# Optimization experiments

Measured on AMD Instinct MI355X. Metric: run time of the kernel, lower is better.

The kernel has to match this reference:

```python
import jax, jax.numpy as jnp
import numpy as np

HIDDEN = 2048
NUM_HEADS = 16
HEAD_DIM = HIDDEN // NUM_HEADS  # 128
SCALE = HEAD_DIM ** -0.5


def setup_inputs() -> dict:
    key = jax.random.key(0)
    ks = jax.random.split(key, 5)
    B, S = 2, 2048
    init = HIDDEN ** -0.5  # roughly kaiming-uniform scale for Linear weights
    return {
        "hidden_states": jax.random.normal(ks[0], (B, S, HIDDEN), dtype=jnp.float32),
        "Wq": jax.random.normal(ks[1], (HIDDEN, HIDDEN), dtype=jnp.float32) * init,
        "Wk": jax.random.normal(ks[2], (HIDDEN, HIDDEN), dtype=jnp.float32) * init,
        "Wv": jax.random.normal(ks[3], (HIDDEN, HIDDEN), dtype=jnp.float32) * init,
        "Wo": jax.random.normal(ks[4], (HIDDEN, HIDDEN), dtype=jnp.float32) * init,
    }


def reference(hidden_states, Wq, Wk, Wv, Wo):
    B, S, _ = hidden_states.shape
    # Projections (nn.Linear: x @ W.T; weights stored as [out, in])
    q = (hidden_states @ Wq.T).reshape(B, S, NUM_HEADS, HEAD_DIM).transpose(0, 2, 1, 3)
    k = (hidden_states @ Wk.T).reshape(B, S, NUM_HEADS, HEAD_DIM).transpose(0, 2, 1, 3)
    v = (hidden_states @ Wv.T).reshape(B, S, NUM_HEADS, HEAD_DIM).transpose(0, 2, 1, 3)
    # Full quadratic attention (faithful to the source's explicit materialization)
    scores = jnp.einsum("bhqd,bhkd->bhqk", q, k) * SCALE  # [B,H,S,S]
    probs = jax.nn.softmax(scores, axis=-1)
    attn = jnp.einsum("bhqk,bhkd->bhqd", probs, v)  # [B,H,S,Dh]
    attn = attn.transpose(0, 2, 1, 3).reshape(B, S, HIDDEN)
    return attn @ Wo.T
```

## Files before the change

kernel.cpp:

```cpp
#include <hip/hip_runtime.h>
#include <cstdint>

#define HIDDEN 2048
#define NHEADS 16
#define DH 128
#define BATCH 2
#define SEQ 2048
#define MTOT 4096
#define BH (BATCH * NHEADS)

typedef __attribute__((ext_vector_type(8))) short bf16x8;
typedef __attribute__((ext_vector_type(4))) float f32x4;

static constexpr float QSCALE = (float)(0.08838834764831845 * 1.4426950408889634);

__device__ __forceinline__ unsigned short f2bf(float f) {
  union { float f; uint32_t u; } v; v.f = f;
  uint32_t r = v.u + 0x7FFFu + ((v.u >> 16) & 1u);
  return (unsigned short)(r >> 16);
}
__device__ __forceinline__ uint32_t cvtpk(float lo, float hi) {
  uint32_t r;
  asm("v_cvt_pk_bf16_f32 %0, %1, %2" : "=v"(r) : "v"(lo), "v"(hi));
  return r;
}
__device__ __forceinline__ f32x4 mfma16(bf16x8 a, bf16x8 b, f32x4 c) {
  return __builtin_amdgcn_mfma_f32_16x16x32_bf16(a, b, c, 0, 0, 0);
}

typedef const __attribute__((address_space(1))) unsigned char* gas1_t;
typedef __attribute__((address_space(3))) unsigned char* las3_t;
__device__ __forceinline__ void gll16(const void* g, void* l) {
  __builtin_amdgcn_global_load_lds((gas1_t)g, (las3_t)l, 16, 0, 0);
}

__global__ __launch_bounds__(256) void cast_all(
    const float* __restrict__ X, const float* __restrict__ Wq,
    const float* __restrict__ Wk, const float* __restrict__ Wv,
    const float* __restrict__ Wo, unsigned short* __restrict__ Xb,
    unsigned short* __restrict__ Wqb, unsigned short* __restrict__ Wkb,
    unsigned short* __restrict__ Wvb, unsigned short* __restrict__ Wob) {
  const int n1 = MTOT * HIDDEN;
  const int i = (blockIdx.x * 256 + threadIdx.x) * 4;
  const float* s;
  unsigned short* d;
  int o;
  if (i < n1) {
    s = X; d = Xb; o = i;
  } else {
    const int j = i - n1;
    const int w = j >> 22;
    o = j & ((1 << 22) - 1);
    s = (w == 0) ? Wq : (w == 1) ? Wk : (w == 2) ? Wv : Wo;
    d = (w == 0) ? Wqb : (w == 1) ? Wkb : (w == 2) ? Wvb : Wob;
  }
  float4 f = *(const float4*)&s[o];
  ushort4 u;
  u.x = f2bf(f.x); u.y = f2bf(f.y); u.z = f2bf(f.z); u.w = f2bf(f.w);
  *(ushort4*)&d[o] = u;
}

template <int VM, bool PF>
__device__ __forceinline__ void qkv3_body(
    int t, char* SM, const unsigned short* aS, const unsigned short* bSq,
    const unsigned short* bSk, const unsigned short* bSv, int wv, int wr,
    int wc, int g, int lr, f32x4 (&accQ)[4][2], f32x4 (&accK)[4][2],
    f32x4 (&accV)[4][2]) {
  const char* slot = SM + (t % 3) * 32768;
  char* slot2 = SM + ((t + 2) % 3) * 32768;
  const size_t ko = (size_t)(t + 2) * 32;
  const int coff = (g ^ ((lr >> 1) & 3)) * 16;
  bf16x8 a[4], bq[2], bk[2], bv[2];
#pragma unroll
  for (int mi = 0; mi < 4; ++mi)
    a[mi] = *(const bf16x8*)(slot + (wr * 64 + mi * 16 + lr) * 64 + coff);
#pragma unroll
  for (int ni = 0; ni < 2; ++ni) {
    const int brow = (wc * 32 + ni * 16 + lr) * 64 + coff;
    bq[ni] = *(const bf16x8*)(slot + 8192 + brow);
    bk[ni] = *(const bf16x8*)(slot + 16384 + brow);
    bv[ni] = *(const bf16x8*)(slot + 24576 + brow);
  }
  if (PF) {
    gll16(aS + ko, slot2 + wv * 1024);
    gll16(bSq + ko, slot2 + 8192 + wv * 1024);
    gll16(bSk + ko, slot2 + 16384 + wv * 1024);
    gll16(bSv + ko, slot2 + 24576 + wv * 1024);
  }
  __builtin_amdgcn_s_setprio(1);
#pragma unroll
  for (int mi = 0; mi < 4; ++mi)
#pragma unroll
    for (int ni = 0; ni < 2; ++ni) {
      accQ[mi][ni] = mfma16(a[mi], bq[ni], accQ[mi][ni]);
      accK[mi][ni] = mfma16(a[mi], bk[ni], accK[mi][ni]);
      accV[mi][ni] = mfma16(a[mi], bv[ni], accV[mi][ni]);
    }
  __builtin_amdgcn_s_setprio(0);
  if (VM == 4) asm volatile("s_waitcnt vmcnt(4)" ::: "memory");
  else if (VM == 0) asm volatile("s_waitcnt vmcnt(0)" ::: "memory");
  if (VM >= 0) __builtin_amdgcn_s_barrier();
}

__global__ __launch_bounds__(512) void gemm_qkv_fused(
    const unsigned short* __restrict__ A, const unsigned short* __restrict__ Wq,
    const unsigned short* __restrict__ Wk, const unsigned short* __restrict__ Wv,
    unsigned short* __restrict__ Qb, unsigned short* __restrict__ Kb,
    unsigned short* __restrict__ Vb) {
  __shared__ __align__(16) char SM[98304];
  const int tid = threadIdx.x;
  const int lane = tid & 63, wv = tid >> 6;
  const int wr = wv >> 2, wc = wv & 3;
  const int g = lane >> 4, lr = lane & 15;
  const int m0 = blockIdx.y * 128, n0 = blockIdx.x * 128;

  const int row0 = tid >> 2, j0 = (tid & 3) ^ ((row0 >> 1) & 3);
  const unsigned short* aS  = A  + (size_t)(m0 + row0) * HIDDEN + j0 * 8;
  const unsigned short* bSq = Wq + (size_t)(n0 + row0) * HIDDEN + j0 * 8;
  const unsigned short* bSk = Wk + (size_t)(n0 + row0) * HIDDEN + j0 * 8;
  const unsigned short* bSv = Wv + (size_t)(n0 + row0) * HIDDEN + j0 * 8;

  f32x4 accQ[4][2], accK[4][2], accV[4][2];
#pragma unroll
  for (int i = 0; i < 4; ++i)
#pragma unroll
    for (int j = 0; j < 2; ++j) {
      accQ[i][j] = (f32x4){0.f, 0.f, 0.f, 0.f};
      accK[i][j] = (f32x4){0.f, 0.f, 0.f, 0.f};
      accV[i][j] = (f32x4){0.f, 0.f, 0.f, 0.f};
    }

#pragma unroll
  for (int tt = 0; tt < 2; ++tt) {
    char* slot = SM + tt * 32768;
    const size_t ko = (size_t)tt * 32;
    gll16(aS + ko, slot + wv * 1024);
    gll16(bSq + ko, slot + 8192 + wv * 1024);
    gll16(bSk + ko, slot + 16384 + wv * 1024);
    gll16(bSv + ko, slot + 24576 + wv * 1024);
  }
  asm volatile("s_waitcnt vmcnt(4)" ::: "memory");
  __builtin_amdgcn_s_barrier();

  for (int t = 0; t < 62; ++t)
    qkv3_body<4, true>(t, SM, aS, bSq, bSk, bSv, wv, wr, wc, g, lr,
                       accQ, accK, accV);
  qkv3_body<0, false>(62, SM, aS, bSq, bSk, bSv, wv, wr, wc, g, lr,
                      accQ, accK, accV);
  qkv3_body<-1, false>(63, SM, aS, bSq, bSk, bSv, wv, wr, wc, g, lr,
                       accQ, accK, accV);

#pragma unroll
  for (int mi = 0; mi < 4; ++mi)
#pragma unroll
    for (int ni = 0; ni < 2; ++ni)
#pragma unroll
      for (int r = 0; r < 4; ++r) {
        const int row = m0 + wr * 64 + mi * 16 + g * 4 + r;
        const int col = n0 + wc * 32 + ni * 16 + lr;
        const int b = row >> 11, s = row & (SEQ - 1);
        const int h = col >> 7, d = col & (DH - 1);
        const size_t base = (size_t)(b * NHEADS + h) * SEQ * DH;
        Qb[base + (size_t)s * DH + d] = f2bf(accQ[mi][ni][r] * QSCALE);
        Kb[base + (size_t)(s >> 5) * 4096 + (d >> 3) * 256 + (s & 31) * 8 + (d & 7)] =
            f2bf(accK[mi][ni][r]);
        Vb[base + (size_t)(s >> 3) * 1024 + d * 8 + (s & 7)] =
            f2bf(accV[mi][ni][r]);
      }
}

template <int VM, bool PF>
__device__ __forceinline__ void pipe_body(
    int kt, char* SM, const unsigned short* aS0, const unsigned short* aS1,
    const unsigned short* bS0, const unsigned short* bS1,
    const unsigned short* bS2, const unsigned short* bS3, int wv, int wr,
    int wc, int g, int lr, f32x4 (&acc)[4][4]) {
  const char* Ac = SM + (kt % 3) * 49152;
  const char* Bc = Ac + 16384;
  char* slot2 = SM + ((kt + 2) % 3) * 49152;
  const size_t ko = (size_t)(kt + 2) * 64;
  const int rx = lr & 7;
  bf16x8 a0[4], b0[4], a1[4], b1[4];
#pragma unroll
  for (int mi = 0; mi < 4; ++mi)
    a0[mi] = *(const bf16x8*)(Ac + (wr * 64 + mi * 16 + lr) * 128 + ((g ^ rx) * 16));
#pragma unroll
  for (int ni = 0; ni < 4; ++ni)
    b0[ni] = *(const bf16x8*)(Bc + (wc * 64 + ni * 16 + lr) * 128 + ((g ^ rx) * 16));
  if (PF) {
    gll16(aS0 + ko, slot2 + wv * 2048);
    gll16(aS1 + ko, slot2 + wv * 2048 + 1024);
    gll16(bS0 + ko, slot2 + 16384 + wv * 4096);
    gll16(bS1 + ko, slot2 + 16384 + wv * 4096 + 1024);
    gll16(bS2 + ko, slot2 + 16384 + wv * 4096 + 2048);
    gll16(bS3 + ko, slot2 + 16384 + wv * 4096 + 3072);
  }
#pragma unroll
  for (int mi = 0; mi < 4; ++mi)
    a1[mi] = *(const bf16x8*)(Ac + (wr * 64 + mi * 16 + lr) * 128 + (((4 + g) ^ rx) * 16));
#pragma unroll
  for (int ni = 0; ni < 4; ++ni)
    b1[ni] = *(const bf16x8*)(Bc + (wc * 64 + ni * 16 + lr) * 128 + (((4 + g) ^ rx) * 16));
  __builtin_amdgcn_s_setprio(1);
#pragma unroll
  for (int mi = 0; mi < 4; ++mi)
#pragma unroll
    for (int ni = 0; ni < 4; ++ni)
      acc[mi][ni] = mfma16(a0[mi], b0[ni], acc[mi][ni]);
#pragma unroll
  for (int mi = 0; mi < 4; ++mi)
#pragma unroll
    for (int ni = 0; ni < 4; ++ni)
      acc[mi][ni] = mfma16(a1[mi], b1[ni], acc[mi][ni]);
  __builtin_amdgcn_s_setprio(0);
  if (VM == 6) asm volatile("s_waitcnt vmcnt(6)" ::: "memory");
  else if (VM == 0) asm volatile("s_waitcnt vmcnt(0)" ::: "memory");
  if (VM >= 0) __builtin_amdgcn_s_barrier();
}

__global__ __launch_bounds__(512) void gemm_out_pipe(
    const unsigned short* __restrict__ A, const unsigned short* __restrict__ W,
    float* __restrict__ C) {
  __shared__ __align__(16) char SM[147456];
  const int tid = threadIdx.x;
  const int lane = tid & 63, wv = tid >> 6;
  const int wr = wv >> 2, wc = wv & 3;
  const int g = lane >> 4, lr = lane & 15;
  const int m0 = blockIdx.y * 128, n0 = blockIdx.x * 256;

  const int idxA0 = wv * 128 + lane, idxA1 = idxA0 + 64;
  const int rA0 = idxA0 >> 3, cA0 = (idxA0 & 7) ^ (rA0 & 7);
  const int rA1 = idxA1 >> 3, cA1 = (idxA1 & 7) ^ (rA1 & 7);
  const unsigned short* aS0 = A + (size_t)(m0 + rA0) * HIDDEN + cA0 * 8;
  const unsigned short* aS1 = A + (size_t)(m0 + rA1) * HIDDEN + cA1 * 8;
  const int idxB0 = wv * 256 + lane, idxB1 = idxB0 + 64,
            idxB2 = idxB0 + 128, idxB3 = idxB0 + 192;
  const int rB0 = idxB0 >> 3, cB0 = (idxB0 & 7) ^ (rB0 & 7);
  const int rB1 = idxB1 >> 3, cB1 = (idxB1 & 7) ^ (rB1 & 7);
  const int rB2 = idxB2 >> 3, cB2 = (idxB2 & 7) ^ (rB2 & 7);
  const int rB3 = idxB3 >> 3, cB3 = (idxB3 & 7) ^ (rB3 & 7);
  const unsigned short* bS0 = W + (size_t)(n0 + rB0) * HIDDEN + cB0 * 8;
  const unsigned short* bS1 = W + (size_t)(n0 + rB1) * HIDDEN + cB1 * 8;
  const unsigned short* bS2 = W + (size_t)(n0 + rB2) * HIDDEN + cB2 * 8;
  const unsigned short* bS3 = W + (size_t)(n0 + rB3) * HIDDEN + cB3 * 8;

  f32x4 acc[4][4];
#pragma unroll
  for (int i = 0; i < 4; ++i)
#pragma unroll
    for (int j = 0; j < 4; ++j) acc[i][j] = (f32x4){0.f, 0.f, 0.f, 0.f};

#pragma unroll
  for (int tt = 0; tt < 2; ++tt) {
    char* slot = SM + tt * 49152;
    const size_t ko = (size_t)tt * 64;
    gll16(aS0 + ko, slot + wv * 2048);
    gll16(aS1 + ko, slot + wv * 2048 + 1024);
    gll16(bS0 + ko, slot + 16384 + wv * 4096);
    gll16(bS1 + ko, slot + 16384 + wv * 4096 + 1024);
    gll16(bS2 + ko, slot + 16384 + wv * 4096 + 2048);
    gll16(bS3 + ko, slot + 16384 + wv * 4096 + 3072);
  }
  asm volatile("s_waitcnt vmcnt(6)" ::: "memory");
  __builtin_amdgcn_s_barrier();

  for (int kt = 0; kt < 30; ++kt)
    pipe_body<6, true>(kt, SM, aS0, aS1, bS0, bS1, bS2, bS3, wv, wr, wc, g,
                       lr, acc);
  pipe_body<0, false>(30, SM, aS0, aS1, bS0, bS1, bS2, bS3, wv, wr, wc, g,
                      lr, acc);
  pipe_body<-1, false>(31, SM, aS0, aS1, bS0, bS1, bS2, bS3, wv, wr, wc, g,
                       lr, acc);

#pragma unroll
  for (int mi = 0; mi < 4; ++mi)
#pragma unroll
    for (int ni = 0; ni < 4; ++ni)
#pragma unroll
      for (int r = 0; r < 4; ++r) {
        const int row = m0 + wr * 64 + mi * 16 + g * 4 + r;
        const int col = n0 + wc * 64 + ni * 16 + lr;
        C[(size_t)row * HIDDEN + col] = acc[mi][ni][r];
      }
}

__global__ __launch_bounds__(256, 4) void attn_mfma(const unsigned short* __restrict__ Q,
                                                    const unsigned short* __restrict__ K,
                                                    const unsigned short* __restrict__ V,
                                                    unsigned short* __restrict__ Ab) {
  const int bid = blockIdx.x;
  const int bh = bid & 31;
  const int q0 = (bid >> 5) * 64;
  const int tid = threadIdx.x;
  const int wv = tid >> 6, lane = tid & 63;
  const int g = lane >> 4, lr = lane & 15;
  const unsigned short* Qh = Q + (size_t)bh * SEQ * DH;
  const unsigned short* Kh = K + (size_t)bh * SEQ * DH;
  const unsigned short* Vh = V + (size_t)bh * SEQ * DH;

  __shared__ __align__(16) unsigned short Kls[2][4096];
  __shared__ __align__(16) unsigned short Vls[2][4096];
  __shared__ __align__(16) unsigned short Pw[4][16][40];

  bf16x8 qf[4];
#pragma unroll
  for (int kb = 0; kb < 4; ++kb)
    qf[kb] = *(const bf16x8*)&Qh[(size_t)(q0 + wv * 16 + lr) * DH + kb * 32 + g * 8];

  f32x4 acc[8];
#pragma unroll
  for (int dn = 0; dn < 8; ++dn) acc[dn] = (f32x4){0.f, 0.f, 0.f, 0.f};
  float mrun = -1e30f;
  float lrun = 0.f;

#pragma unroll
  for (int j = 0; j < 2; ++j) {
    const int c = j * 256 + tid;
    gll16(Kh + (size_t)c * 8, (char*)&Kls[0][0] + j * 4096 + wv * 1024);
    gll16(Vh + (size_t)c * 8, (char*)&Vls[0][0] + j * 4096 + wv * 1024);
  }

  for (int t = 0; t < 64; ++t) {
    const int cur = t & 1;
    asm volatile("s_waitcnt vmcnt(0)" ::: "memory");
    __builtin_amdgcn_s_barrier();
    if (t + 1 < 64) {
      const unsigned short* Kn = Kh + (size_t)(t + 1) * 4096;
      const unsigned short* Vn = Vh + (size_t)(t + 1) * 4096;
      char* kd = (char*)&Kls[cur ^ 1][0];
      char* vd = (char*)&Vls[cur ^ 1][0];
#pragma unroll
      for (int j = 0; j < 2; ++j) {
        const int c = j * 256 + tid;
        gll16(Kn + (size_t)c * 8, kd + j * 4096 + wv * 1024);
        gll16(Vn + (size_t)c * 8, vd + j * 4096 + wv * 1024);
      }
    }

    const char* Kc = (const char*)&Kls[cur][0];
    const char* Vc = (const char*)&Vls[cur][0];

    f32x4 st0 = (f32x4){0.f, 0.f, 0.f, 0.f};
    f32x4 st1 = (f32x4){0.f, 0.f, 0.f, 0.f};
    __builtin_amdgcn_s_setprio(1);
#pragma unroll
    for (int kb = 0; kb < 4; ++kb) {
      const int cb = (kb * 4 + g) * 32;
      bf16x8 kf0 = *(const bf16x8*)(Kc + (cb + lr) * 16);
      bf16x8 kf1 = *(const bf16x8*)(Kc + (cb + 16 + lr) * 16);
      st0 = mfma16(kf0, qf[kb], st0);
      st1 = mfma16(kf1, qf[kb], st1);
    }
    __builtin_amdgcn_s_setprio(0);
    float mt = fmaxf(fmaxf(fmaxf(st0[0], st0[1]), fmaxf(st0[2], st0[3])),
                     fmaxf(fmaxf(st1[0], st1[1]), fmaxf(st1[2], st1[3])));
    mt = fmaxf(mt, __shfl_xor(mt, 16));
    mt = fmaxf(mt, __shfl_xor(mt, 32));
    if (!__all(mt <= mrun + 8.0f)) {
      const float mnew = fmaxf(mrun, mt);
      const float corr = __builtin_amdgcn_exp2f(mrun - mnew);
      lrun *= corr;
      mrun = mnew;
      const f32x4 cv = (f32x4){__shfl(corr, g * 4 + 0), __shfl(corr, g * 4 + 1),
                               __shfl(corr, g * 4 + 2), __shfl(corr, g * 4 + 3)};
#pragma unroll
      for (int dn = 0; dn < 8; ++dn) acc[dn] *= cv;
    }
    float p[8], ls = 0.f;
#pragma unroll
    for (int r = 0; r < 4; ++r) {
      p[r] = __builtin_amdgcn_exp2f(st0[r] - mrun);
      p[4 + r] = __builtin_amdgcn_exp2f(st1[r] - mrun);
      ls += p[r] + p[4 + r];
    }
    lrun += ls;
    uint2 pk0, pk1;
    pk0.x = cvtpk(p[0], p[1]); pk0.y = cvtpk(p[2], p[3]);
    pk1.x = cvtpk(p[4], p[5]); pk1.y = cvtpk(p[6], p[7]);
    *(uint2*)&Pw[wv][lr][4 * g] = pk0;
    *(uint2*)&Pw[wv][lr][16 + 4 * g] = pk1;
    bf16x8 ap = *(const bf16x8*)&Pw[wv][lr][8 * g];
    __builtin_amdgcn_s_setprio(1);
#pragma unroll
    for (int dn = 0; dn < 8; ++dn) {
      bf16x8 vf = *(const bf16x8*)(Vc + (g * 128 + dn * 16 + lr) * 16);
      acc[dn] = mfma16(ap, vf, acc[dn]);
    }
    __builtin_amdgcn_s_setprio(0);
  }

  const int b = bh >> 4, h = bh & 15;
  lrun += __shfl_xor(lrun, 16);
  lrun += __shfl_xor(lrun, 32);
  const float inv = 1.f / lrun;
  float ir[4];
#pragma unroll
  for (int r = 0; r < 4; ++r) ir[r] = __shfl(inv, g * 4 + r);
#pragma unroll
  for (int dn = 0; dn < 8; ++dn)
#pragma unroll
    for (int r = 0; r < 4; ++r) {
      const int srow = q0 + wv * 16 + g * 4 + r;
      Ab[((size_t)(b * SEQ + srow) * NHEADS + h) * DH + dn * 16 + lr] =
          f2bf(acc[dn][r] * ir[r]);
    }
}

extern "C" void kernel_launch(void* const* d_in, const int* in_sizes, int n_in,
                              void* d_out, int out_size, void* d_ws,
                              size_t ws_size, hipStream_t stream) {
  const float* X  = (const float*)d_in[0];
  const float* Wq = (const float*)d_in[1];
  const float* Wk = (const float*)d_in[2];
  const float* Wv = (const float*)d_in[3];
  const float* Wo = (const float*)d_in[4];
  float* out = (float*)d_out;

  const int n1 = MTOT * HIDDEN;
  const int n2 = HIDDEN * HIDDEN;

  char* p = (char*)d_ws;
  unsigned short* Xb  = (unsigned short*)(p + 0);
  unsigned short* Qb  = (unsigned short*)(p + 16777216);
  unsigned short* Kb  = (unsigned short*)(p + 33554432);
  unsigned short* Vb  = (unsigned short*)(p + 50331648);
  unsigned short* Wqb = (unsigned short*)(p + 67108864);
  unsigned short* Wkb = (unsigned short*)(p + 75497472);
  unsigned short* Wvb = (unsigned short*)(p + 83886080);
  unsigned short* Wob = (unsigned short*)(p + 92274688);
  unsigned short* Ab  = (unsigned short*)(p + 100663296);

  cast_all<<<(n1 + 4 * n2) / 1024, 256, 0, stream>>>(X, Wq, Wk, Wv, Wo, Xb, Wqb,
                                                     Wkb, Wvb, Wob);

  gemm_qkv_fused<<<dim3(HIDDEN / 128, MTOT / 128), 512, 0, stream>>>(
      Xb, Wqb, Wkb, Wvb, Qb, Kb, Vb);

  attn_mfma<<<dim3(1024), 256, 0, stream>>>(Qb, Kb, Vb, Ab);

  gemm_out_pipe<<<dim3(HIDDEN / 256, MTOT / 128), 512, 0, stream>>>(Ab, Wob, out);
}
```

Measured before the change: 272.0 us.

## Switch QKV GEMM from triple-buffered to double-buffered LDS pipeline

Replaces the three-slot LDS ring with prefetch distance two by a simple two-slot double buffer that prefetches one K-tile ahead. Shared memory per block drops from 96KB to 64KB, which may allow more blocks per CU. The cost is a full vmcnt(0) wait and a barrier at the top of every iteration, so global load latency is hidden less.

```diff
diff --git a/kernel.cpp b/kernel.cpp
--- a/kernel.cpp
+++ b/kernel.cpp
@@ -60,54 +60,12 @@
   *(ushort4*)&d[o] = u;
 }
 
-template <int VM, bool PF>
-__device__ __forceinline__ void qkv3_body(
-    int t, char* SM, const unsigned short* aS, const unsigned short* bSq,
-    const unsigned short* bSk, const unsigned short* bSv, int wv, int wr,
-    int wc, int g, int lr, f32x4 (&accQ)[4][2], f32x4 (&accK)[4][2],
-    f32x4 (&accV)[4][2]) {
-  const char* slot = SM + (t % 3) * 32768;
-  char* slot2 = SM + ((t + 2) % 3) * 32768;
-  const size_t ko = (size_t)(t + 2) * 32;
-  const int coff = (g ^ ((lr >> 1) & 3)) * 16;
-  bf16x8 a[4], bq[2], bk[2], bv[2];
-#pragma unroll
-  for (int mi = 0; mi < 4; ++mi)
-    a[mi] = *(const bf16x8*)(slot + (wr * 64 + mi * 16 + lr) * 64 + coff);
-#pragma unroll
-  for (int ni = 0; ni < 2; ++ni) {
-    const int brow = (wc * 32 + ni * 16 + lr) * 64 + coff;
-    bq[ni] = *(const bf16x8*)(slot + 8192 + brow);
-    bk[ni] = *(const bf16x8*)(slot + 16384 + brow);
-    bv[ni] = *(const bf16x8*)(slot + 24576 + brow);
-  }
-  if (PF) {
-    gll16(aS + ko, slot2 + wv * 1024);
-    gll16(bSq + ko, slot2 + 8192 + wv * 1024);
-    gll16(bSk + ko, slot2 + 16384 + wv * 1024);
-    gll16(bSv + ko, slot2 + 24576 + wv * 1024);
-  }
-  __builtin_amdgcn_s_setprio(1);
-#pragma unroll
-  for (int mi = 0; mi < 4; ++mi)
-#pragma unroll
-    for (int ni = 0; ni < 2; ++ni) {
-      accQ[mi][ni] = mfma16(a[mi], bq[ni], accQ[mi][ni]);
-      accK[mi][ni] = mfma16(a[mi], bk[ni], accK[mi][ni]);
-      accV[mi][ni] = mfma16(a[mi], bv[ni], accV[mi][ni]);
-    }
-  __builtin_amdgcn_s_setprio(0);
-  if (VM == 4) asm volatile("s_waitcnt vmcnt(4)" ::: "memory");
-  else if (VM == 0) asm volatile("s_waitcnt vmcnt(0)" ::: "memory");
-  if (VM >= 0) __builtin_amdgcn_s_barrier();
-}
-
 __global__ __launch_bounds__(512) void gemm_qkv_fused(
     const unsigned short* __restrict__ A, const unsigned short* __restrict__ Wq,
     const unsigned short* __restrict__ Wk, const unsigned short* __restrict__ Wv,
     unsigned short* __restrict__ Qb, unsigned short* __restrict__ Kb,
     unsigned short* __restrict__ Vb) {
-  __shared__ __align__(16) char SM[98304];
+  __shared__ __align__(16) char SM[65536];
   const int tid = threadIdx.x;
   const int lane = tid & 63, wv = tid >> 6;
   const int wr = wv >> 2, wc = wv & 3;
@@ -130,25 +88,46 @@
       accV[i][j] = (f32x4){0.f, 0.f, 0.f, 0.f};
     }
 
-#pragma unroll
-  for (int tt = 0; tt < 2; ++tt) {
-    char* slot = SM + tt * 32768;
-    const size_t ko = (size_t)tt * 32;
-    gll16(aS + ko, slot + wv * 1024);
-    gll16(bSq + ko, slot + 8192 + wv * 1024);
-    gll16(bSk + ko, slot + 16384 + wv * 1024);
-    gll16(bSv + ko, slot + 24576 + wv * 1024);
-  }
-  asm volatile("s_waitcnt vmcnt(4)" ::: "memory");
-  __builtin_amdgcn_s_barrier();
-
-  for (int t = 0; t < 62; ++t)
-    qkv3_body<4, true>(t, SM, aS, bSq, bSk, bSv, wv, wr, wc, g, lr,
-                       accQ, accK, accV);
-  qkv3_body<0, false>(62, SM, aS, bSq, bSk, bSv, wv, wr, wc, g, lr,
-                      accQ, accK, accV);
-  qkv3_body<-1, false>(63, SM, aS, bSq, bSk, bSv, wv, wr, wc, g, lr,
-                       accQ, accK, accV);
+  gll16(aS, SM + wv * 1024);
+  gll16(bSq, SM + 8192 + wv * 1024);
+  gll16(bSk, SM + 16384 + wv * 1024);
+  gll16(bSv, SM + 24576 + wv * 1024);
+
+  const int coff = (g ^ ((lr >> 1) & 3)) * 16;
+  for (int t = 0; t < 64; ++t) {
+    const char* slot = SM + (t & 1) * 32768;
+    asm volatile("s_waitcnt vmcnt(0)" ::: "memory");
+    __builtin_amdgcn_s_barrier();
+    if (t + 1 < 64) {
+      char* nslot = SM + ((t + 1) & 1) * 32768;
+      const size_t ko = (size_t)(t + 1) * 32;
+      gll16(aS + ko, nslot + wv * 1024);
+      gll16(bSq + ko, nslot + 8192 + wv * 1024);
+      gll16(bSk + ko, nslot + 16384 + wv * 1024);
+      gll16(bSv + ko, nslot + 24576 + wv * 1024);
+    }
+    bf16x8 a[4], bq[2], bk[2], bv[2];
+#pragma unroll
+    for (int mi = 0; mi < 4; ++mi)
+      a[mi] = *(const bf16x8*)(slot + (wr * 64 + mi * 16 + lr) * 64 + coff);
+#pragma unroll
+    for (int ni = 0; ni < 2; ++ni) {
+      const int brow = (wc * 32 + ni * 16 + lr) * 64 + coff;
+      bq[ni] = *(const bf16x8*)(slot + 8192 + brow);
+      bk[ni] = *(const bf16x8*)(slot + 16384 + brow);
+      bv[ni] = *(const bf16x8*)(slot + 24576 + brow);
+    }
+    __builtin_amdgcn_s_setprio(1);
+#pragma unroll
+    for (int mi = 0; mi < 4; ++mi)
+#pragma unroll
+      for (int ni = 0; ni < 2; ++ni) {
+        accQ[mi][ni] = mfma16(a[mi], bq[ni], accQ[mi][ni]);
+        accK[mi][ni] = mfma16(a[mi], bk[ni], accK[mi][ni]);
+        accV[mi][ni] = mfma16(a[mi], bv[ni], accV[mi][ni]);
+      }
+    __builtin_amdgcn_s_setprio(0);
+  }
 
 #pragma unroll
   for (int mi = 0; mi < 4; ++mi)
```

Result: no change. 271.0 us (-0.4%).
